# Kernel optimization log

Measured on AMD Instinct MI355X. Metric: run time of the kernel, lower is better.

Reference implementation:

```python
import jax, jax.numpy as jnp
import numpy as np


def _ln(x, g, b, eps=1e-5):
    m = jnp.mean(x, axis=-1, keepdims=True)
    v = jnp.mean((x - m) ** 2, axis=-1, keepdims=True)
    return (x - m) / jnp.sqrt(v + eps) * g + b


def _win_part(x, ws):
    # (B,H,W,C) -> (B*nW, ws*ws, C)
    B, H, W, C = x.shape
    x = x.reshape(B, H // ws, ws, W // ws, ws, C)
    x = jnp.transpose(x, (0, 1, 3, 2, 4, 5))
    return x.reshape(-1, ws * ws, C)


def _win_rev(w, ws, H, W):
    # (B*nW, ws, ws, C) -> (B,H,W,C)
    C = w.shape[-1]
    B = w.shape[0] // ((H // ws) * (W // ws))
    x = w.reshape(B, H // ws, W // ws, ws, ws, C)
    x = jnp.transpose(x, (0, 1, 3, 2, 4, 5))
    return x.reshape(B, H, W, C)


def _build_mask(H, W, ws, ss):
    # standard Swin SW-MSA mask, built with numpy at trace time (static shapes)
    img = np.zeros((H, W), np.float32)
    cnt = 0
    for hs in (slice(0, -ws), slice(-ws, -ss), slice(-ss, None)):
        for wsl in (slice(0, -ws), slice(-ws, -ss), slice(-ss, None)):
            img[hs, wsl] = cnt
            cnt += 1
    mw = img.reshape(H // ws, ws, W // ws, ws).transpose(0, 2, 1, 3).reshape(-1, ws * ws)
    diff = mw[:, None, :] - mw[:, :, None]  # (nW, N, N)
    return jnp.asarray(np.where(diff != 0, -np.inf, 0.0).astype(np.float32))


def _swin_block(x, H, W, ws, shift, heads, p):
    B, L, C = x.shape
    hd = C // heads
    N = ws * ws
    shortcut = x
    xg = _ln(x, p['ln1_g'], p['ln1_b']).reshape(B, H, W, C)
    mask = None
    if shift > 0:
        xg = jnp.roll(xg, shift=(-shift, -shift), axis=(1, 2))
        mask = _build_mask(H, W, ws, shift)
    xw = _win_part(xg, ws)  # (B_, N, C)
    qkv = xw @ p['qkv_w'] + p['qkv_b']  # (B_, N, 3C)
    qkv = jnp.transpose(qkv.reshape(-1, N, 3, heads, hd), (2, 0, 3, 1, 4))
    q, k, v = qkv[0] * (hd ** -0.5), qkv[1], qkv[2]  # (B_, h, N, hd)
    attn = jnp.einsum('bhnd,bhmd->bhnm', q, k)
    if mask is not None:
        nW = mask.shape[0]
        attn = attn.reshape(B, nW, heads, N, N) + mask[None, :, None]
        attn = attn.reshape(-1, heads, N, N)
    attn = jax.nn.softmax(attn, axis=-1)
    out = jnp.einsum('bhnm,bhmd->bhnd', attn, v)
    out = jnp.transpose(out, (0, 2, 1, 3)).reshape(-1, N, C)
    out = out @ p['proj_w'] + p['proj_b']
    xg = _win_rev(out.reshape(-1, ws, ws, C), ws, H, W)
    if shift > 0:
        xg = jnp.roll(xg, shift=(shift, shift), axis=(1, 2))
    x = shortcut + xg.reshape(B, L, C)
    h = jax.nn.gelu(_ln(x, p['ln2_g'], p['ln2_b']) @ p['fc1_w'] + p['fc1_b'], approximate=False)
    return x + (h @ p['fc2_w'] + p['fc2_b'])


def _patch_merge(x, H, W, g, b, w):
    B, L, C = x.shape
    xg = x.reshape(B, H, W, C)
    xc = jnp.concatenate([xg[:, 0::2, 0::2], xg[:, 1::2, 0::2], xg[:, 0::2, 1::2], xg[:, 1::2, 1::2]], axis=-1)
    xc = xc.reshape(B, (H // 2) * (W // 2), 4 * C)
    return _ln(xc, g, b) @ w


def setup_inputs() -> dict:
    key = jax.random.key(0)
    ks = jax.random.split(key, 16)
    B, H, W, C = 8, 96, 96, 128
    s = 0.02
    d = {'x': jax.random.normal(ks[0], (B, H * W, C), jnp.float32)}
    i = 1
    for pre in ('a_', 'b_'):
        d[pre + 'ln1_g'] = jnp.ones((C,), jnp.float32)
        d[pre + 'ln1_b'] = jnp.zeros((C,), jnp.float32)
        d[pre + 'qkv_w'] = s * jax.random.normal(ks[i], (C, 3 * C), jnp.float32); i += 1
        d[pre + 'qkv_b'] = jnp.zeros((3 * C,), jnp.float32)
        d[pre + 'proj_w'] = s * jax.random.normal(ks[i], (C, C), jnp.float32); i += 1
        d[pre + 'proj_b'] = jnp.zeros((C,), jnp.float32)
        d[pre + 'ln2_g'] = jnp.ones((C,), jnp.float32)
        d[pre + 'ln2_b'] = jnp.zeros((C,), jnp.float32)
        d[pre + 'fc1_w'] = s * jax.random.normal(ks[i], (C, 4 * C), jnp.float32); i += 1
        d[pre + 'fc1_b'] = jnp.zeros((4 * C,), jnp.float32)
        d[pre + 'fc2_w'] = s * jax.random.normal(ks[i], (4 * C, C), jnp.float32); i += 1
        d[pre + 'fc2_b'] = jnp.zeros((C,), jnp.float32)
    d['mln_g'] = jnp.ones((4 * C,), jnp.float32)
    d['mln_b'] = jnp.zeros((4 * C,), jnp.float32)
    d['red_w'] = s * jax.random.normal(ks[i], (4 * C, 2 * C), jnp.float32)
    d['H'] = H
    d['W'] = W
    return d


def reference(x, a_ln1_g, a_ln1_b, a_qkv_w, a_qkv_b, a_proj_w, a_proj_b, a_ln2_g, a_ln2_b, a_fc1_w, a_fc1_b, a_fc2_w, a_fc2_b, b_ln1_g, b_ln1_b, b_qkv_w, b_qkv_b, b_proj_w, b_proj_b, b_ln2_g, b_ln2_b, b_fc1_w, b_fc1_b, b_fc2_w, b_fc2_b, mln_g, mln_b, red_w, H, W):
    heads, ws = 4, 8
    pa = dict(ln1_g=a_ln1_g, ln1_b=a_ln1_b, qkv_w=a_qkv_w, qkv_b=a_qkv_b, proj_w=a_proj_w, proj_b=a_proj_b, ln2_g=a_ln2_g, ln2_b=a_ln2_b, fc1_w=a_fc1_w, fc1_b=a_fc1_b, fc2_w=a_fc2_w, fc2_b=a_fc2_b)
    pb = dict(ln1_g=b_ln1_g, ln1_b=b_ln1_b, qkv_w=b_qkv_w, qkv_b=b_qkv_b, proj_w=b_proj_w, proj_b=b_proj_b, ln2_g=b_ln2_g, ln2_b=b_ln2_b, fc1_w=b_fc1_w, fc1_b=b_fc1_b, fc2_w=b_fc2_w, fc2_b=b_fc2_b)
    x = _swin_block(x, H, W, ws, 0, heads, pa)          # W-MSA
    x = _swin_block(x, H, W, ws, ws // 2, heads, pb)     # SW-MSA
    return _patch_merge(x, H, W, mln_g, mln_b, red_w)    # (B, HW/4, 2C)
```

## Files before the change

kernel.cpp:

```cpp
#include <hip/hip_runtime.h>
#include <hip/hip_bf16.h>

typedef __bf16 bf16_t;
typedef __bf16 bf16x2 __attribute__((ext_vector_type(2)));
typedef __bf16 bf16x8 __attribute__((ext_vector_type(8)));
typedef float floatx4 __attribute__((ext_vector_type(4)));

#define NTOK 73728

__device__ __forceinline__ void gl16(const bf16_t* g, bf16_t* l) {
    __builtin_amdgcn_global_load_lds((const __attribute__((address_space(1))) void*)g,
                                     (__attribute__((address_space(3))) void*)l, 16, 0, 0);
}

__device__ __forceinline__ void stage128x128(const bf16_t* src, size_t srcStride, bf16_t* lds, int tid) {
    #pragma unroll
    for (int i = 0; i < 8; i++) {
        int c = i * 256 + tid;
        int p = c >> 9;
        int row = (c >> 2) & 127;
        int seg = c & 3;
        gl16(src + (size_t)row * srcStride + p * 32 + seg * 8, lds + c * 8);
    }
}

__device__ __forceinline__ void stage_ln(const float* __restrict__ src, const float* __restrict__ g,
                                         const float* __restrict__ bta, bf16_t* lnA, int tid) {
    int r = tid >> 2, q = tid & 3;
    const float* rowp = src + (size_t)r * 128 + q * 32;
    float4 v[8];
    float s = 0.0f, sq = 0.0f;
    #pragma unroll
    for (int i = 0; i < 8; i++) {
        v[i] = *(const float4*)(rowp + i * 4);
        s += v[i].x + v[i].y + v[i].z + v[i].w;
        sq += v[i].x * v[i].x + v[i].y * v[i].y + v[i].z * v[i].z + v[i].w * v[i].w;
    }
    s += __shfl_xor(s, 1, 64); sq += __shfl_xor(sq, 1, 64);
    s += __shfl_xor(s, 2, 64); sq += __shfl_xor(sq, 2, 64);
    float m = s * (1.0f / 128.0f);
    float inv = rsqrtf(sq * (1.0f / 128.0f) - m * m + 1e-5f);
    bf16_t* dst = lnA + q * 2048 + r * 32;
    #pragma unroll
    for (int i = 0; i < 4; i++) {
        float4 a = v[2 * i], b = v[2 * i + 1];
        float4 g0 = *(const float4*)(g + q * 32 + i * 8);
        float4 g1 = *(const float4*)(g + q * 32 + i * 8 + 4);
        float4 b0 = *(const float4*)(bta + q * 32 + i * 8);
        float4 b1 = *(const float4*)(bta + q * 32 + i * 8 + 4);
        bf16x8 o;
        o[0] = (bf16_t)((a.x - m) * inv * g0.x + b0.x);
        o[1] = (bf16_t)((a.y - m) * inv * g0.y + b0.y);
        o[2] = (bf16_t)((a.z - m) * inv * g0.z + b0.z);
        o[3] = (bf16_t)((a.w - m) * inv * g0.w + b0.w);
        o[4] = (bf16_t)((b.x - m) * inv * g1.x + b1.x);
        o[5] = (bf16_t)((b.y - m) * inv * g1.y + b1.y);
        o[6] = (bf16_t)((b.z - m) * inv * g1.z + b1.z);
        o[7] = (bf16_t)((b.w - m) * inv * g1.w + b1.w);
        *(bf16x8*)(dst + i * 8) = o;
    }
}

struct TPack {
    const float* src[9];
    bf16_t* dst[9];
    int K[9], N[9];
};
__global__ __launch_bounds__(256) void kconv_t9(TPack p) {
    int seg = blockIdx.y;
    int K = p.K[seg], N = p.N[seg];
    int idx = blockIdx.x * 256 + threadIdx.x;
    if (idx >= K * N) return;
    int n = idx / K, k = idx - n * K;
    p.dst[seg][idx] = (bf16_t)p.src[seg][k * N + n];
}

__global__ __launch_bounds__(256, 3) void kqkv(const float* __restrict__ X,
                                               const float* __restrict__ g, const float* __restrict__ bta,
                                               const bf16_t* __restrict__ Wt,
                                               const float* __restrict__ bias,
                                               bf16_t* __restrict__ out) {
    alignas(16) __shared__ bf16_t lA[64 * 128];
    alignas(16) __shared__ bf16_t lB[128 * 128];
    const int tid = threadIdx.x;
    const int rowA = blockIdx.y * 64;
    const int rowB = blockIdx.x * 128;
    stage_ln(X + (size_t)rowA * 128, g, bta, lA, tid);
    stage128x128(Wt + (size_t)rowB * 128, 128, lB, tid);
    __syncthreads();
    const int lane = tid & 63, wv = tid >> 6;
    const int wm = (wv & 1) * 32, wn = (wv >> 1) * 64;
    const int frow = lane & 15, fq = lane >> 4;
    floatx4 acc[2][4] = {};
    #pragma unroll
    for (int kc = 0; kc < 4; kc++) {
        bf16x8 af[2], bfr[4];
        #pragma unroll
        for (int i = 0; i < 2; i++)
            af[i] = *(const bf16x8*)&lA[kc * 2048 + (wm + i * 16 + frow) * 32 + fq * 8];
        #pragma unroll
        for (int j = 0; j < 4; j++)
            bfr[j] = *(const bf16x8*)&lB[kc * 4096 + (wn + j * 16 + frow) * 32 + fq * 8];
        #pragma unroll
        for (int i = 0; i < 2; i++)
            #pragma unroll
            for (int j = 0; j < 4; j++)
                acc[i][j] = __builtin_amdgcn_mfma_f32_16x16x32_bf16(af[i], bfr[j], acc[i][j], 0, 0, 0);
    }
    #pragma unroll
    for (int i = 0; i < 2; i++)
        #pragma unroll
        for (int j = 0; j < 4; j++) {
            int col = rowB + wn + j * 16 + frow;
            float bs = bias[col];
            #pragma unroll
            for (int r = 0; r < 4; r++) {
                int row = rowA + wm + i * 16 + fq * 4 + r;
                out[(size_t)row * 384 + col] = (bf16_t)(acc[i][j][r] + bs);
            }
        }
}

__global__ __launch_bounds__(256, 2) void kmlp(float* __restrict__ res,
                                               const float* __restrict__ g, const float* __restrict__ bta,
                                               const bf16_t* __restrict__ W1t,
                                               const float* __restrict__ b1,
                                               const bf16_t* __restrict__ W2t,
                                               const float* __restrict__ b2) {
    alignas(16) __shared__ bf16_t lA[64 * 128];
    alignas(16) __shared__ bf16_t lW[128 * 128];
    alignas(16) __shared__ bf16_t lH[64 * 128];
    const int tid = threadIdx.x;
    const int rowA = blockIdx.x * 64;
    const int lane = tid & 63, wv = tid >> 6;
    const int wm = (wv & 1) * 32, wn = (wv >> 1) * 64;
    const int frow = lane & 15, fq = lane >> 4;
    stage_ln(res + (size_t)rowA * 128, g, bta, lA, tid);
    floatx4 accO[2][4] = {};
    for (int cn = 0; cn < 4; cn++) {
        __syncthreads();
        stage128x128(W1t + (size_t)(cn * 128) * 128, 128, lW, tid);
        __syncthreads();
        floatx4 accH[2][4] = {};
        #pragma unroll
        for (int kc = 0; kc < 4; kc++) {
            bf16x8 af[2], bfr[4];
            #pragma unroll
            for (int i = 0; i < 2; i++)
                af[i] = *(const bf16x8*)&lA[kc * 2048 + (wm + i * 16 + frow) * 32 + fq * 8];
            #pragma unroll
            for (int j = 0; j < 4; j++)
                bfr[j] = *(const bf16x8*)&lW[kc * 4096 + (wn + j * 16 + frow) * 32 + fq * 8];
            #pragma unroll
            for (int i = 0; i < 2; i++)
                #pragma unroll
                for (int j = 0; j < 4; j++)
                    accH[i][j] = __builtin_amdgcn_mfma_f32_16x16x32_bf16(af[i], bfr[j], accH[i][j], 0, 0, 0);
        }
        #pragma unroll
        for (int j = 0; j < 4; j++) {
            int col = wn + j * 16 + frow;
            float bs = b1[cn * 128 + col];
            #pragma unroll
            for (int i = 0; i < 2; i++)
                #pragma unroll
                for (int r = 0; r < 4; r++) {
                    int row = wm + i * 16 + fq * 4 + r;
                    float v = accH[i][j][r] + bs;
                    float u = 1.5957691216057308f * (v + 0.044715f * v * v * v);
                    lH[(col >> 5) * 2048 + row * 32 + (col & 31)] = (bf16_t)(v / (1.0f + __expf(-u)));
                }
        }
        __syncthreads();
        stage128x128(W2t + cn * 128, 512, lW, tid);
        __syncthreads();
        #pragma unroll
        for (int kc = 0; kc < 4; kc++) {
            bf16x8 af[2], bfr[4];
            #pragma unroll
            for (int i = 0; i < 2; i++)
                af[i] = *(const bf16x8*)&lH[kc * 2048 + (wm + i * 16 + frow) * 32 + fq * 8];
            #pragma unroll
            for (int j = 0; j < 4; j++)
                bfr[j] = *(const bf16x8*)&lW[kc * 4096 + (wn + j * 16 + frow) * 32 + fq * 8];
            #pragma unroll
            for (int i = 0; i < 2; i++)
                #pragma unroll
                for (int j = 0; j < 4; j++)
                    accO[i][j] = __builtin_amdgcn_mfma_f32_16x16x32_bf16(af[i], bfr[j], accO[i][j], 0, 0, 0);
        }
    }
    #pragma unroll
    for (int j = 0; j < 4; j++) {
        int col = wn + j * 16 + frow;
        float bs = b2[col];
        #pragma unroll
        for (int i = 0; i < 2; i++)
            #pragma unroll
            for (int r = 0; r < 4; r++) {
                int row = rowA + wm + i * 16 + fq * 4 + r;
                size_t off = (size_t)row * 128 + col;
                res[off] = res[off] + accO[i][j][r] + bs;
            }
    }
}

template<int MODE>
__global__ __launch_bounds__(256, 5) void gemm64x128(const bf16_t* __restrict__ A,
                                                     const bf16_t* __restrict__ Bt,
                                                     const float* __restrict__ bias,
                                                     const float* __restrict__ res,
                                                     float* __restrict__ outf,
                                                     bf16_t* __restrict__ outh,
                                                     int M, int N, int K) {
    alignas(16) __shared__ bf16_t lA[2 * 64 * 32];
    alignas(16) __shared__ bf16_t lB[2 * 128 * 32];
    const int tid = threadIdx.x;
    const int lane = tid & 63;
    const int wv = tid >> 6;
    const int wm = (wv & 1) * 32;
    const int wn = (wv >> 1) * 64;
    const int frow = lane & 15, fq = lane >> 4;
    const int rowA = blockIdx.y * 64;
    const int rowB = blockIdx.x * 128;
    const int sr = tid >> 2, sc = (tid & 3) * 8;
    const bf16_t* pa = A + (size_t)(rowA + sr) * K + sc;
    const bf16_t* pb0 = Bt + (size_t)(rowB + sr) * K + sc;
    const bf16_t* pb1 = Bt + (size_t)(rowB + 64 + sr) * K + sc;
    floatx4 acc[2][4] = {};
    for (int k0 = 0; k0 < K; k0 += 64) {
        __syncthreads();
        gl16(pa  + k0,      &lA[tid * 8]);
        gl16(pa  + k0 + 32, &lA[2048 + tid * 8]);
        gl16(pb0 + k0,      &lB[tid * 8]);
        gl16(pb1 + k0,      &lB[2048 + tid * 8]);
        gl16(pb0 + k0 + 32, &lB[4096 + tid * 8]);
        gl16(pb1 + k0 + 32, &lB[4096 + 2048 + tid * 8]);
        __syncthreads();
        #pragma unroll
        for (int s = 0; s < 2; s++) {
            bf16x8 af[2], bfr[4];
            #pragma unroll
            for (int i = 0; i < 2; i++)
                af[i] = *(const bf16x8*)&lA[s * 2048 + (wm + i * 16 + frow) * 32 + fq * 8];
            #pragma unroll
            for (int j = 0; j < 4; j++)
                bfr[j] = *(const bf16x8*)&lB[s * 4096 + (wn + j * 16 + frow) * 32 + fq * 8];
            #pragma unroll
            for (int i = 0; i < 2; i++)
                #pragma unroll
                for (int j = 0; j < 4; j++)
                    acc[i][j] = __builtin_amdgcn_mfma_f32_16x16x32_bf16(af[i], bfr[j], acc[i][j], 0, 0, 0);
        }
    }
    #pragma unroll
    for (int i = 0; i < 2; i++) {
        #pragma unroll
        for (int j = 0; j < 4; j++) {
            int col = rowB + wn + j * 16 + frow;
            float bs = (MODE == 3) ? 0.0f : bias[col];
            #pragma unroll
            for (int r = 0; r < 4; r++) {
                int row = rowA + wm + i * 16 + fq * 4 + r;
                float v = acc[i][j][r] + bs;
                size_t off = (size_t)row * N + col;
                if (MODE == 1) {
                    outf[off] = res[off] + v;
                } else {
                    outf[off] = v;
                }
            }
        }
    }
}

__global__ __launch_bounds__(256) void kmergeln(const float* __restrict__ x, const float* __restrict__ g,
                                                const float* __restrict__ bta, bf16_t* __restrict__ out) {
    int row = blockIdx.x * 4 + (threadIdx.x >> 6);
    int lane = threadIdx.x & 63;
    int b = row / 2304; int rr = row - b * 2304;
    int i2 = rr / 48, j2 = rr - i2 * 48;
    int q = lane >> 4;
    int cc = (lane & 15) * 8;
    int di = q & 1, dj = q >> 1;
    int src = ((b * 96 + i2 * 2 + di) * 96 + (j2 * 2 + dj)) * 128 + cc;
    float4 a0 = *(const float4*)&x[src];
    float4 a1 = *(const float4*)&x[src + 4];
    float s  = a0.x + a0.y + a0.z + a0.w + a1.x + a1.y + a1.z + a1.w;
    float sq = a0.x*a0.x + a0.y*a0.y + a0.z*a0.z + a0.w*a0.w
             + a1.x*a1.x + a1.y*a1.y + a1.z*a1.z + a1.w*a1.w;
    #pragma unroll
    for (int d = 1; d < 64; d <<= 1) { s += __shfl_xor(s, d, 64); sq += __shfl_xor(sq, d, 64); }
    float m = s * (1.0f / 512.0f);
    float var = sq * (1.0f / 512.0f) - m * m;
    float inv = 1.0f / sqrtf(var + 1e-5f);
    int c = q * 128 + cc;
    float4 g0 = *(const float4*)&g[c];
    float4 g1 = *(const float4*)&g[c + 4];
    float4 b0 = *(const float4*)&bta[c];
    float4 b1 = *(const float4*)&bta[c + 4];
    bf16x8 o;
    o[0] = (bf16_t)((a0.x - m) * inv * g0.x + b0.x);
    o[1] = (bf16_t)((a0.y - m) * inv * g0.y + b0.y);
    o[2] = (bf16_t)((a0.z - m) * inv * g0.z + b0.z);
    o[3] = (bf16_t)((a0.w - m) * inv * g0.w + b0.w);
    o[4] = (bf16_t)((a1.x - m) * inv * g1.x + b1.x);
    o[5] = (bf16_t)((a1.y - m) * inv * g1.y + b1.y);
    o[6] = (bf16_t)((a1.z - m) * inv * g1.z + b1.z);
    o[7] = (bf16_t)((a1.w - m) * inv * g1.w + b1.w);
    *(bf16x8*)&out[row * 512 + c] = o;
}

__global__ __launch_bounds__(64) void kattn(const bf16_t* __restrict__ qkv, bf16_t* __restrict__ out, int shift) {
    alignas(16) __shared__ bf16_t lp[64 * 64];
    alignas(16) __shared__ bf16_t lv[64 * 32];
    int blk = blockIdx.x;
    int win = blk >> 2, h = blk & 3;
    int b = win / 144; int wr = win - b * 144;
    int wi = wr / 12, wj = wr - wi * 12;
    int ri0 = wi * 8, rj0 = wj * 8;
    int lane = threadIdx.x;
    auto trow = [&](int n) {
        int oi = ri0 + (n >> 3) + shift; oi = (oi >= 96) ? oi - 96 : oi;
        int oj = rj0 + (n & 7) + shift;  oj = (oj >= 96) ? oj - 96 : oj;
        return (b * 96 + oi) * 96 + oj;
    };
    {
        size_t base = (size_t)trow(lane) * 384 + 256 + h * 32;
        *(uint4*)&lv[lane * 32]      = *(const uint4*)&qkv[base];
        *(uint4*)&lv[lane * 32 + 8]  = *(const uint4*)&qkv[base + 8];
        *(uint4*)&lv[lane * 32 + 16] = *(const uint4*)&qkv[base + 16];
        *(uint4*)&lv[lane * 32 + 24] = *(const uint4*)&qkv[base + 24];
    }
    int frow = lane & 15, fk = (lane >> 4) * 8;
    bf16x8 qf[4], kf[4];
    #pragma unroll
    for (int t = 0; t < 4; t++) {
        size_t rq = (size_t)trow(t * 16 + frow) * 384;
        qf[t] = *(const bf16x8*)&qkv[rq + h * 32 + fk];
        kf[t] = *(const bf16x8*)&qkv[rq + 128 + h * 32 + fk];
    }
    floatx4 S[4][4] = {};
    #pragma unroll
    for (int mt = 0; mt < 4; mt++)
        #pragma unroll
        for (int nt = 0; nt < 4; nt++)
            S[mt][nt] = __builtin_amdgcn_mfma_f32_16x16x32_bf16(qf[mt], kf[nt], S[mt][nt], 0, 0, 0);
    const float scale = 0.17677669529663687f;
    #pragma unroll
    for (int mt = 0; mt < 4; mt++)
        #pragma unroll
        for (int nt = 0; nt < 4; nt++)
            #pragma unroll
            for (int r = 0; r < 4; r++) S[mt][nt][r] *= scale;
    if (shift > 0) {
        auto grpn = [&](int n) {
            int ri = ri0 + (n >> 3), rj = rj0 + (n & 7);
            int gr = (ri < 88) ? 0 : ((ri < 92) ? 1 : 2);
            int gc = (rj < 88) ? 0 : ((rj < 92) ? 1 : 2);
            return gr * 3 + gc;
        };
        int gk[4];
        #pragma unroll
        for (int nt = 0; nt < 4; nt++) gk[nt] = grpn(nt * 16 + frow);
        #pragma unroll
        for (int mt = 0; mt < 4; mt++)
            #pragma unroll
            for (int r = 0; r < 4; r++) {
                int gq = grpn(mt * 16 + (lane >> 4) * 4 + r);
                #pragma unroll
                for (int nt = 0; nt < 4; nt++)
                    if (gq != gk[nt]) S[mt][nt][r] = -1e30f;
            }
    }
    #pragma unroll
    for (int mt = 0; mt < 4; mt++) {
        #pragma unroll
        for (int r = 0; r < 4; r++) {
            float mx = fmaxf(fmaxf(S[mt][0][r], S[mt][1][r]), fmaxf(S[mt][2][r], S[mt][3][r]));
            #pragma unroll
            for (int d = 1; d < 16; d <<= 1) mx = fmaxf(mx, __shfl_xor(mx, d, 64));
            float sm = 0.0f;
            #pragma unroll
            for (int nt = 0; nt < 4; nt++) {
                float p = __expf(S[mt][nt][r] - mx);
                S[mt][nt][r] = p;
                sm += p;
            }
            #pragma unroll
            for (int d = 1; d < 16; d <<= 1) sm += __shfl_xor(sm, d, 64);
            float inv = 1.0f / sm;
            #pragma unroll
            for (int nt = 0; nt < 4; nt++) S[mt][nt][r] *= inv;
        }
    }
    #pragma unroll
    for (int mt = 0; mt < 4; mt++)
        #pragma unroll
        for (int nt = 0; nt < 4; nt++)
            #pragma unroll
            for (int r = 0; r < 4; r++)
                lp[(mt * 16 + (lane >> 4) * 4 + r) * 64 + nt * 16 + frow] = (bf16_t)S[mt][nt][r];
    __syncthreads();
    floatx4 O[4][2] = {};
    #pragma unroll
    for (int ks = 0; ks < 2; ks++) {
        bf16x8 vbs[2];
        #pragma unroll
        for (int nt = 0; nt < 2; nt++)
            #pragma unroll
            for (int j = 0; j < 8; j++)
                vbs[nt][j] = lv[(ks * 32 + fk + j) * 32 + nt * 16 + frow];
        #pragma unroll
        for (int mt = 0; mt < 4; mt++) {
            bf16x8 pa = *(const bf16x8*)&lp[(mt * 16 + frow) * 64 + ks * 32 + fk];
            #pragma unroll
            for (int nt = 0; nt < 2; nt++)
                O[mt][nt] = __builtin_amdgcn_mfma_f32_16x16x32_bf16(pa, vbs[nt], O[mt][nt], 0, 0, 0);
        }
    }
    #pragma unroll
    for (int mt = 0; mt < 4; mt++) {
        #pragma unroll
        for (int r = 0; r < 4; r++) {
            int qr = mt * 16 + (lane >> 4) * 4 + r;
            size_t orow = (size_t)trow(qr) * 128 + h * 32;
            #pragma unroll
            for (int nt = 0; nt < 2; nt++)
                out[orow + nt * 16 + frow] = (bf16_t)O[mt][nt][r];
        }
    }
}

extern "C" void kernel_launch(void* const* d_in, const int* in_sizes, int n_in,
                              void* d_out, int out_size, void* d_ws, size_t ws_size,
                              hipStream_t stream) {
    const float* x       = (const float*)d_in[0];
    const float* a_ln1g  = (const float*)d_in[1];
    const float* a_ln1b  = (const float*)d_in[2];
    const float* a_qkvw  = (const float*)d_in[3];
    const float* a_qkvb  = (const float*)d_in[4];
    const float* a_projw = (const float*)d_in[5];
    const float* a_projb = (const float*)d_in[6];
    const float* a_ln2g  = (const float*)d_in[7];
    const float* a_ln2b  = (const float*)d_in[8];
    const float* a_fc1w  = (const float*)d_in[9];
    const float* a_fc1b  = (const float*)d_in[10];
    const float* a_fc2w  = (const float*)d_in[11];
    const float* a_fc2b  = (const float*)d_in[12];
    const float* b_ln1g  = (const float*)d_in[13];
    const float* b_ln1b  = (const float*)d_in[14];
    const float* b_qkvw  = (const float*)d_in[15];
    const float* b_qkvb  = (const float*)d_in[16];
    const float* b_projw = (const float*)d_in[17];
    const float* b_projb = (const float*)d_in[18];
    const float* b_ln2g  = (const float*)d_in[19];
    const float* b_ln2b  = (const float*)d_in[20];
    const float* b_fc1w  = (const float*)d_in[21];
    const float* b_fc1b  = (const float*)d_in[22];
    const float* b_fc2w  = (const float*)d_in[23];
    const float* b_fc2b  = (const float*)d_in[24];
    const float* mlng    = (const float*)d_in[25];
    const float* mlnb    = (const float*)d_in[26];
    const float* redw    = (const float*)d_in[27];
    float* out = (float*)d_out;

    char* p = (char*)d_ws;
    float*  buf_x   = (float*)p;  p += (size_t)NTOK * 128 * 4;
    bf16_t* buf_qkv = (bf16_t*)p; p += (size_t)NTOK * 384 * 2;
    bf16_t* buf_attn= (bf16_t*)p; p += (size_t)NTOK * 128 * 2;
    bf16_t* buf_mrg = (bf16_t*)p; p += (size_t)18432 * 512 * 2;
    bf16_t* wt      = (bf16_t*)p;
    bf16_t* aqkvT  = wt;
    bf16_t* aprojT = aqkvT  + 384 * 128;
    bf16_t* afc1T  = aprojT + 128 * 128;
    bf16_t* afc2T  = afc1T  + 512 * 128;
    bf16_t* bqkvT  = afc2T  + 128 * 512;
    bf16_t* bprojT = bqkvT  + 384 * 128;
    bf16_t* bfc1T  = bprojT + 128 * 128;
    bf16_t* bfc2T  = bfc1T  + 512 * 128;
    bf16_t* redT   = bfc2T  + 128 * 512;

    TPack tp;
    const float* srcs[9] = {a_qkvw, a_projw, a_fc1w, a_fc2w, b_qkvw, b_projw, b_fc1w, b_fc2w, redw};
    bf16_t* dsts[9] = {aqkvT, aprojT, afc1T, afc2T, bqkvT, bprojT, bfc1T, bfc2T, redT};
    int Ks[9] = {128, 128, 128, 512, 128, 128, 128, 512, 512};
    int Ns[9] = {384, 128, 512, 128, 384, 128, 512, 128, 256};
    for (int i = 0; i < 9; i++) { tp.src[i] = srcs[i]; tp.dst[i] = dsts[i]; tp.K[i] = Ks[i]; tp.N[i] = Ns[i]; }
    kconv_t9<<<dim3(512, 9), dim3(256), 0, stream>>>(tp);

    const dim3 blk256(256);
    const int MG = NTOK / 64;

    kqkv<<<dim3(3, MG), blk256, 0, stream>>>(x, a_ln1g, a_ln1b, aqkvT, a_qkvb, buf_qkv);
    kattn<<<dim3(1152 * 4), dim3(64), 0, stream>>>(buf_qkv, buf_attn, 0);
    gemm64x128<1><<<dim3(1, MG), blk256, 0, stream>>>(buf_attn, aprojT, a_projb, x, buf_x, nullptr, NTOK, 128, 128);
    kmlp<<<dim3(MG), blk256, 0, stream>>>(buf_x, a_ln2g, a_ln2b, afc1T, a_fc1b, afc2T, a_fc2b);

    kqkv<<<dim3(3, MG), blk256, 0, stream>>>(buf_x, b_ln1g, b_ln1b, bqkvT, b_qkvb, buf_qkv);
    kattn<<<dim3(1152 * 4), dim3(64), 0, stream>>>(buf_qkv, buf_attn, 4);
    gemm64x128<1><<<dim3(1, MG), blk256, 0, stream>>>(buf_attn, bprojT, b_projb, buf_x, buf_x, nullptr, NTOK, 128, 128);
    kmlp<<<dim3(MG), blk256, 0, stream>>>(buf_x, b_ln2g, b_ln2b, bfc1T, b_fc1b, bfc2T, b_fc2b);

    kmergeln<<<dim3(18432 / 4), blk256, 0, stream>>>(buf_x, mlng, mlnb, buf_mrg);
    gemm64x128<3><<<dim3(2, 288), blk256, 0, stream>>>(buf_mrg, redT, nullptr, nullptr, out, nullptr, 18432, 256, 512);
}
```

Measured before the change: 476.9 us.

## Load weight fragments directly from global memory instead of staging in LDS

The qkv, MLP and projection/reduction GEMMs no longer stage weight tiles into shared memory. Each wave reads its B fragments straight from global memory, relying on L1/L2 caching of the small weight matrices. This removes LDS traffic, a pair of barriers per MLP chunk, and LDS footprint; the LN and hidden tiles switch to a row-major layout padded to 136 to avoid bank conflicts. Launch-bound occupancy hints are raised for qkv and MLP and lowered for the GEMM. The risk is higher global-load latency on the MFMA critical path and more, uncoalesced cache traffic per wave.

```diff
diff --git a/kernel.cpp b/kernel.cpp
--- a/kernel.cpp
+++ b/kernel.cpp
@@ -7,21 +7,11 @@
 typedef float floatx4 __attribute__((ext_vector_type(4)));
 
 #define NTOK 73728
+#define LNS 136
 
 __device__ __forceinline__ void gl16(const bf16_t* g, bf16_t* l) {
     __builtin_amdgcn_global_load_lds((const __attribute__((address_space(1))) void*)g,
                                      (__attribute__((address_space(3))) void*)l, 16, 0, 0);
-}
-
-__device__ __forceinline__ void stage128x128(const bf16_t* src, size_t srcStride, bf16_t* lds, int tid) {
-    #pragma unroll
-    for (int i = 0; i < 8; i++) {
-        int c = i * 256 + tid;
-        int p = c >> 9;
-        int row = (c >> 2) & 127;
-        int seg = c & 3;
-        gl16(src + (size_t)row * srcStride + p * 32 + seg * 8, lds + c * 8);
-    }
 }
 
 __device__ __forceinline__ void stage_ln(const float* __restrict__ src, const float* __restrict__ g,
@@ -40,7 +30,7 @@
     s += __shfl_xor(s, 2, 64); sq += __shfl_xor(sq, 2, 64);
     float m = s * (1.0f / 128.0f);
     float inv = rsqrtf(sq * (1.0f / 128.0f) - m * m + 1e-5f);
-    bf16_t* dst = lnA + q * 2048 + r * 32;
+    bf16_t* dst = lnA + r * LNS + q * 32;
     #pragma unroll
     for (int i = 0; i < 4; i++) {
         float4 a = v[2 * i], b = v[2 * i + 1];
@@ -75,32 +65,31 @@
     p.dst[seg][idx] = (bf16_t)p.src[seg][k * N + n];
 }
 
-__global__ __launch_bounds__(256, 3) void kqkv(const float* __restrict__ X,
+__global__ __launch_bounds__(256, 4) void kqkv(const float* __restrict__ X,
                                                const float* __restrict__ g, const float* __restrict__ bta,
                                                const bf16_t* __restrict__ Wt,
                                                const float* __restrict__ bias,
                                                bf16_t* __restrict__ out) {
-    alignas(16) __shared__ bf16_t lA[64 * 128];
-    alignas(16) __shared__ bf16_t lB[128 * 128];
+    alignas(16) __shared__ bf16_t lA[64 * LNS];
     const int tid = threadIdx.x;
     const int rowA = blockIdx.y * 64;
     const int rowB = blockIdx.x * 128;
     stage_ln(X + (size_t)rowA * 128, g, bta, lA, tid);
-    stage128x128(Wt + (size_t)rowB * 128, 128, lB, tid);
     __syncthreads();
     const int lane = tid & 63, wv = tid >> 6;
     const int wm = (wv & 1) * 32, wn = (wv >> 1) * 64;
     const int frow = lane & 15, fq = lane >> 4;
+    const bf16_t* pw = Wt + (size_t)(rowB + wn + frow) * 128 + fq * 8;
     floatx4 acc[2][4] = {};
     #pragma unroll
     for (int kc = 0; kc < 4; kc++) {
         bf16x8 af[2], bfr[4];
         #pragma unroll
         for (int i = 0; i < 2; i++)
-            af[i] = *(const bf16x8*)&lA[kc * 2048 + (wm + i * 16 + frow) * 32 + fq * 8];
+            af[i] = *(const bf16x8*)&lA[(wm + i * 16 + frow) * LNS + kc * 32 + fq * 8];
         #pragma unroll
         for (int j = 0; j < 4; j++)
-            bfr[j] = *(const bf16x8*)&lB[kc * 4096 + (wn + j * 16 + frow) * 32 + fq * 8];
+            bfr[j] = *(const bf16x8*)(pw + (size_t)j * 16 * 128 + kc * 32);
         #pragma unroll
         for (int i = 0; i < 2; i++)
             #pragma unroll
@@ -121,36 +110,35 @@
         }
 }
 
-__global__ __launch_bounds__(256, 2) void kmlp(float* __restrict__ res,
+__global__ __launch_bounds__(256, 3) void kmlp(float* __restrict__ res,
                                                const float* __restrict__ g, const float* __restrict__ bta,
                                                const bf16_t* __restrict__ W1t,
                                                const float* __restrict__ b1,
                                                const bf16_t* __restrict__ W2t,
                                                const float* __restrict__ b2) {
-    alignas(16) __shared__ bf16_t lA[64 * 128];
-    alignas(16) __shared__ bf16_t lW[128 * 128];
-    alignas(16) __shared__ bf16_t lH[64 * 128];
+    alignas(16) __shared__ bf16_t lA[64 * LNS];
+    alignas(16) __shared__ bf16_t lH[64 * LNS];
     const int tid = threadIdx.x;
     const int rowA = blockIdx.x * 64;
     const int lane = tid & 63, wv = tid >> 6;
     const int wm = (wv & 1) * 32, wn = (wv >> 1) * 64;
     const int frow = lane & 15, fq = lane >> 4;
     stage_ln(res + (size_t)rowA * 128, g, bta, lA, tid);
+    const bf16_t* pw1 = W1t + (size_t)(wn + frow) * 128 + fq * 8;
+    const bf16_t* pw2 = W2t + (size_t)(wn + frow) * 512 + fq * 8;
     floatx4 accO[2][4] = {};
     for (int cn = 0; cn < 4; cn++) {
         __syncthreads();
-        stage128x128(W1t + (size_t)(cn * 128) * 128, 128, lW, tid);
-        __syncthreads();
         floatx4 accH[2][4] = {};
         #pragma unroll
         for (int kc = 0; kc < 4; kc++) {
             bf16x8 af[2], bfr[4];
             #pragma unroll
             for (int i = 0; i < 2; i++)
-                af[i] = *(const bf16x8*)&lA[kc * 2048 + (wm + i * 16 + frow) * 32 + fq * 8];
+                af[i] = *(const bf16x8*)&lA[(wm + i * 16 + frow) * LNS + kc * 32 + fq * 8];
             #pragma unroll
             for (int j = 0; j < 4; j++)
-                bfr[j] = *(const bf16x8*)&lW[kc * 4096 + (wn + j * 16 + frow) * 32 + fq * 8];
+                bfr[j] = *(const bf16x8*)(pw1 + (size_t)(cn * 128 + j * 16) * 128 + kc * 32);
             #pragma unroll
             for (int i = 0; i < 2; i++)
                 #pragma unroll
@@ -168,21 +156,19 @@
                     int row = wm + i * 16 + fq * 4 + r;
                     float v = accH[i][j][r] + bs;
                     float u = 1.5957691216057308f * (v + 0.044715f * v * v * v);
-                    lH[(col >> 5) * 2048 + row * 32 + (col & 31)] = (bf16_t)(v / (1.0f + __expf(-u)));
+                    lH[row * LNS + col] = (bf16_t)(v / (1.0f + __expf(-u)));
                 }
         }
-        __syncthreads();
-        stage128x128(W2t + cn * 128, 512, lW, tid);
         __syncthreads();
         #pragma unroll
         for (int kc = 0; kc < 4; kc++) {
             bf16x8 af[2], bfr[4];
             #pragma unroll
             for (int i = 0; i < 2; i++)
-                af[i] = *(const bf16x8*)&lH[kc * 2048 + (wm + i * 16 + frow) * 32 + fq * 8];
+                af[i] = *(const bf16x8*)&lH[(wm + i * 16 + frow) * LNS + kc * 32 + fq * 8];
             #pragma unroll
             for (int j = 0; j < 4; j++)
-                bfr[j] = *(const bf16x8*)&lW[kc * 4096 + (wn + j * 16 + frow) * 32 + fq * 8];
+                bfr[j] = *(const bf16x8*)(pw2 + (size_t)(j * 16) * 512 + cn * 128 + kc * 32);
             #pragma unroll
             for (int i = 0; i < 2; i++)
                 #pragma unroll
@@ -206,15 +192,13 @@
 }
 
 template<int MODE>
-__global__ __launch_bounds__(256, 5) void gemm64x128(const bf16_t* __restrict__ A,
+__global__ __launch_bounds__(256, 4) void gemm64x128(const bf16_t* __restrict__ A,
                                                      const bf16_t* __restrict__ Bt,
                                                      const float* __restrict__ bias,
                                                      const float* __restrict__ res,
                                                      float* __restrict__ outf,
-                                                     bf16_t* __restrict__ outh,
                                                      int M, int N, int K) {
     alignas(16) __shared__ bf16_t lA[2 * 64 * 32];
-    alignas(16) __shared__ bf16_t lB[2 * 128 * 32];
     const int tid = threadIdx.x;
     const int lane = tid & 63;
     const int wv = tid >> 6;
@@ -225,17 +209,12 @@
     const int rowB = blockIdx.x * 128;
     const int sr = tid >> 2, sc = (tid & 3) * 8;
     const bf16_t* pa = A + (size_t)(rowA + sr) * K + sc;
-    const bf16_t* pb0 = Bt + (size_t)(rowB + sr) * K + sc;
-    const bf16_t* pb1 = Bt + (size_t)(rowB + 64 + sr) * K + sc;
+    const bf16_t* pb = Bt + (size_t)(rowB + wn + frow) * K + fq * 8;
     floatx4 acc[2][4] = {};
     for (int k0 = 0; k0 < K; k0 += 64) {
         __syncthreads();
-        gl16(pa  + k0,      &lA[tid * 8]);
-        gl16(pa  + k0 + 32, &lA[2048 + tid * 8]);
-        gl16(pb0 + k0,      &lB[tid * 8]);
-        gl16(pb1 + k0,      &lB[2048 + tid * 8]);
-        gl16(pb0 + k0 + 32, &lB[4096 + tid * 8]);
-        gl16(pb1 + k0 + 32, &lB[4096 + 2048 + tid * 8]);
+        gl16(pa + k0,      &lA[tid * 8]);
+        gl16(pa + k0 + 32, &lA[2048 + tid * 8]);
         __syncthreads();
         #pragma unroll
         for (int s = 0; s < 2; s++) {
@@ -245,7 +224,7 @@
                 af[i] = *(const bf16x8*)&lA[s * 2048 + (wm + i * 16 + frow) * 32 + fq * 8];
             #pragma unroll
             for (int j = 0; j < 4; j++)
-                bfr[j] = *(const bf16x8*)&lB[s * 4096 + (wn + j * 16 + frow) * 32 + fq * 8];
+                bfr[j] = *(const bf16x8*)(pb + (size_t)j * 16 * K + k0 + s * 32);
             #pragma unroll
             for (int i = 0; i < 2; i++)
                 #pragma unroll
@@ -494,14 +473,14 @@
 
     kqkv<<<dim3(3, MG), blk256, 0, stream>>>(x, a_ln1g, a_ln1b, aqkvT, a_qkvb, buf_qkv);
     kattn<<<dim3(1152 * 4), dim3(64), 0, stream>>>(buf_qkv, buf_attn, 0);
-    gemm64x128<1><<<dim3(1, MG), blk256, 0, stream>>>(buf_attn, aprojT, a_projb, x, buf_x, nullptr, NTOK, 128, 128);
+    gemm64x128<1><<<dim3(1, MG), blk256, 0, stream>>>(buf_attn, aprojT, a_projb, x, buf_x, NTOK, 128, 128);
     kmlp<<<dim3(MG), blk256, 0, stream>>>(buf_x, a_ln2g, a_ln2b, afc1T, a_fc1b, afc2T, a_fc2b);
 
     kqkv<<<dim3(3, MG), blk256, 0, stream>>>(buf_x, b_ln1g, b_ln1b, bqkvT, b_qkvb, buf_qkv);
     kattn<<<dim3(1152 * 4), dim3(64), 0, stream>>>(buf_qkv, buf_attn, 4);
-    gemm64x128<1><<<dim3(1, MG), blk256, 0, stream>>>(buf_attn, bprojT, b_projb, buf_x, buf_x, nullptr, NTOK, 128, 128);
+    gemm64x128<1><<<dim3(1, MG), blk256, 0, stream>>>(buf_attn, bprojT, b_projb, buf_x, buf_x, NTOK, 128, 128);
     kmlp<<<dim3(MG), blk256, 0, stream>>>(buf_x, b_ln2g, b_ln2b, bfc1T, b_fc1b, bfc2T, b_fc2b);
 
     kmergeln<<<dim3(18432 / 4), blk256, 0, stream>>>(buf_x, mlng, mlnb, buf_mrg);
-    gemm64x128<3><<<dim3(2, 288), blk256, 0, stream>>>(buf_mrg, redT, nullptr, nullptr, out, nullptr, 18432, 256, 512);
-}
+    gemm64x128<3><<<dim3(2, 288), blk256, 0, stream>>>(buf_mrg, redT, nullptr, nullptr, out, 18432, 256, 512);
+}
```

After: 593.7 us. 1.24x slower.
